# Kernel tuning notes

Hardware: AMD Instinct MI355X
Metric: run time of the kernel (lower is better)

Reference implementation:

```python
import jax, jax.numpy as jnp
import numpy as np

N_TOKENS = 3
EMBED = 10
RNN = 10
N_LABELS = 3
B = 16384
T = 99
EPS = 1e-7  # keras CategoricalCrossentropy clip epsilon


def setup_inputs() -> dict:
    key = jax.random.key(0)
    ks = jax.random.split(key, 8)
    token_ids = jax.random.randint(ks[0], (B, T), 0, N_TOKENS, dtype=jnp.int32)
    label_ids = jax.random.randint(ks[1], (B, T), 0, N_LABELS)
    labels = jax.nn.one_hot(label_ids, N_LABELS, dtype=jnp.float32)
    mask = jnp.ones((B, T), dtype=bool)  # accepted by call() but unused, kept for signature fidelity
    emb_table = jax.random.normal(ks[2], (N_TOKENS, EMBED), jnp.float32) * 0.05
    W = jax.random.normal(ks[3], (EMBED, RNN), jnp.float32) / np.sqrt(EMBED)
    U = jax.random.normal(ks[4], (RNN, RNN), jnp.float32) / np.sqrt(RNN)
    b = jnp.zeros((RNN,), jnp.float32)
    Wo = jax.random.normal(ks[5], (RNN, N_LABELS), jnp.float32) / np.sqrt(RNN)
    bo = jnp.zeros((N_LABELS,), jnp.float32)
    return dict(token_ids=token_ids, labels=labels, mask=mask,
                emb_table=emb_table, W=W, U=U, b=b, Wo=Wo, bo=bo)


def reference(token_ids, labels, mask, emb_table, W, U, b, Wo, bo):
    # Embedding lookup (mask_zero=True -> token 0 is a masked step)
    emb = emb_table[token_ids]                      # [B, T, E]
    step_mask = (token_ids != 0)                    # [B, T]

    def step(h, inp):
        x_t, m_t = inp                              # [B, E], [B]
        h_new = jnp.tanh(x_t @ W + h @ U + b)       # SimpleRNN cell
        # Keras masking: masked timesteps carry previous state/output
        h = jnp.where(m_t[:, None], h_new, h)
        return h, h

    h0 = jnp.zeros((token_ids.shape[0], W.shape[1]), emb.dtype)
    _, states_tb = jax.lax.scan(step, h0, (emb.transpose(1, 0, 2), step_mask.T))
    states = states_tb.transpose(1, 0, 2)           # [B, T, R]

    probs = jax.nn.softmax(states @ Wo + bo, axis=-1)   # Dense(softmax) -> [B, T, L]
    probs_c = jnp.clip(probs, EPS, 1.0)
    loss = jnp.mean(-jnp.sum(labels * jnp.log(probs_c), axis=-1))
    accuracy = jnp.mean((jnp.argmax(probs, axis=-1) == jnp.argmax(labels, axis=-1)).astype(jnp.float32))
    return states, probs, accuracy, loss
```

## Files before the change

### kernel.cpp

```cpp
#include <hip/hip_runtime.h>
#include <math.h>

#define BB 16384
#define TT 99
#define RR 10
#define LL 3
#define TILE 33
#define RPW 8
#define WPB 4

#define QP(v, j) __int_as_float(__builtin_amdgcn_mov_dpp(                     \
    __float_as_int(v), (j) * 0x55, 0xF, 0xF, true))
#define HMIR(v)  __int_as_float(__builtin_amdgcn_mov_dpp(                     \
    __float_as_int(v), 0x141, 0xF, 0xF, true))

__device__ __forceinline__ float fast_tanh(float x) {
    float e = __expf(2.0f * x);
    return fmaf(-2.0f, __builtin_amdgcn_rcpf(e + 1.0f), 1.0f);
}

__global__ __launch_bounds__(256, 2)
void rnn_fused_kernel(const int* __restrict__ tok_ids,
                      const float* __restrict__ labels,
                      const float* __restrict__ emb,
                      const float* __restrict__ W,
                      const float* __restrict__ U,
                      const float* __restrict__ bvec,
                      const float* __restrict__ Wo,
                      const float* __restrict__ bo,
                      float* __restrict__ states_out,
                      float* __restrict__ probs_out,
                      float* __restrict__ ws)
{
    __shared__ __align__(16) float          s_st[WPB][RPW * TILE * RR];
    __shared__                unsigned char s_code[WPB][RPW * 100];

    const int tid = threadIdx.x;
    const int w   = tid >> 6;
    const int l   = tid & 63;
    const int r8  = l >> 3;
    const int g   = l & 7;
    const int rowbase = blockIdx.x * (WPB * RPW) + w * RPW;

#pragma unroll 1
    for (int i = 0; i < 13; ++i) {
        const int p = l + 64 * i;
        if (p < RPW * TT) {
            const size_t gi = (size_t)rowbase * TT + p;
            const int   tk  = tok_ids[gi];
            const float la1 = labels[gi * LL + 1];
            const float la2 = labels[gi * LL + 2];
            const int   y   = (la1 > 0.5f) ? 1 : ((la2 > 0.5f) ? 2 : 0);
            const int   r   = p / TT;
            s_code[w][r * 100 + (p - r * TT)] = (unsigned char)((tk << 2) | y);
        }
    }

    const int qpar = g >> 2;
    int ord[8];
#pragma unroll
    for (int j = 0; j < 4; ++j) {
        ord[j]     = qpar ? 4 + j : j;
        ord[4 + j] = qpar ? 3 - j : 7 - j;
    }
    const int jA = g;
    const int jB = ((g & 3) < 2) ? 8 + (g & 3) : 8;

    float UA[RR], UB[RR];
#pragma unroll
    for (int k2 = 0; k2 < 8; ++k2) {
        UA[k2] = U[ord[k2] * RR + jA];
        UB[k2] = U[ord[k2] * RR + jB];
    }
    UA[8] = U[8 * RR + jA]; UA[9] = U[9 * RR + jA];
    UB[8] = U[8 * RR + jB]; UB[9] = U[9 * RR + jB];

    float cA1 = bvec[jA], cA2 = cA1, cB1 = bvec[jB], cB2 = cB1;
#pragma unroll
    for (int i = 0; i < RR; ++i) {
        const float e1 = emb[RR + i];
        const float e2 = emb[2 * RR + i];
        const float wA = W[i * RR + jA];
        const float wB = W[i * RR + jB];
        cA1 = fmaf(e1, wA, cA1); cA2 = fmaf(e2, wA, cA2);
        cB1 = fmaf(e1, wB, cB1); cB2 = fmaf(e2, wB, cB2);
    }

    float hoA = 0.0f, hoB = 0.0f;
    float loss = 0.0f;
    int   corr = 0;
    int code = (int)s_code[w][r8 * 100];

#pragma unroll 1
    for (int k = 0; k < 3; ++k) {
#pragma unroll 1
        for (int tt = 0; tt < TILE; ++tt) {
            const int t   = k * TILE + tt;
            const int cur = code;
            const int tn  = (t + 1 < TT) ? t + 1 : t;
            code = (int)s_code[w][r8 * 100 + tn];
            const int sel = cur >> 2;

            float hg[RR];
            hg[0] = QP(hoA, 0); hg[1] = QP(hoA, 1);
            hg[2] = QP(hoA, 2); hg[3] = QP(hoA, 3);
            const float mr = HMIR(hoA);
            hg[4] = QP(mr, 0);  hg[5] = QP(mr, 1);
            hg[6] = QP(mr, 2);  hg[7] = QP(mr, 3);
            hg[8] = QP(hoB, 0); hg[9] = QP(hoB, 1);

            const bool is1 = (sel == 1);
            float aA0 = is1 ? cA1 : cA2, aB0 = is1 ? cB1 : cB2;
            float aA1 = 0.0f, aB1 = 0.0f;
#pragma unroll
            for (int i = 0; i < 5; ++i) {
                aA0 = fmaf(hg[i],     UA[i],     aA0);
                aA1 = fmaf(hg[5 + i], UA[5 + i], aA1);
                aB0 = fmaf(hg[i],     UB[i],     aB0);
                aB1 = fmaf(hg[5 + i], UB[5 + i], aB1);
            }
            const float hnA = fast_tanh(aA0 + aA1);
            const float hnB = fast_tanh(aB0 + aB1);
            if (sel != 0) { hoA = hnA; hoB = hnB; }

            float* sp = &s_st[w][(r8 * TILE + tt) * RR];
            sp[g] = hoA;
            if (g < 2) sp[8 + g] = hoB;
        }

#pragma unroll 1
        for (int i = 0; i < 21; ++i) {
            const int p = l + 64 * i;
            if (p < 1320) {
                const int r = p / 165;
                const int m = p - r * 165;
                const float2 v = *reinterpret_cast<const float2*>(
                    &s_st[w][r * (TILE * RR) + 2 * m]);
                *reinterpret_cast<float2*>(
                    &states_out[(size_t)(rowbase + r) * (TT * RR)
                                + (size_t)k * (TILE * RR) + 2 * m]) = v;
            }
        }

#pragma unroll 1
        for (int i = 0; i < 5; ++i) {
            const int p = l + 64 * i;
            if (p < RPW * TILE) {
                const int r  = p / TILE;
                const int t2 = p - r * TILE;
                const size_t idx = (size_t)(rowbase + r) * TT + k * TILE + t2;

                const float* hp = &s_st[w][(r * TILE + t2) * RR];
                float h0[RR];
#pragma unroll
                for (int j = 0; j < RR; j += 2) {
                    const float2 v = *reinterpret_cast<const float2*>(hp + j);
                    h0[j] = v.x; h0[j + 1] = v.y;
                }
                float l0 = bo[0], l1 = bo[1], l2 = bo[2];
#pragma unroll
                for (int j = 0; j < RR; ++j) {
                    l0 = fmaf(h0[j], Wo[j * LL + 0], l0);
                    l1 = fmaf(h0[j], Wo[j * LL + 1], l1);
                    l2 = fmaf(h0[j], Wo[j * LL + 2], l2);
                }
                const float e0 = __expf(l0), e1 = __expf(l1), e2 = __expf(l2);
                const float S  = e0 + e1 + e2;
                const float rs = __builtin_amdgcn_rcpf(S);
                probs_out[idx * LL + 0] = e0 * rs;
                probs_out[idx * LL + 1] = e1 * rs;
                probs_out[idx * LL + 2] = e2 * rs;

                const int y = (int)s_code[w][r * 100 + k * TILE + t2] & 3;

                const float ly = (y == 0) ? l0 : ((y == 1) ? l1 : l2);
                loss += fminf(__logf(S) - ly, 16.11809565f);

                int ap = 0; float pm = l0;
                if (l1 > pm) { ap = 1; pm = l1; }
                if (l2 > pm) { ap = 2; }
                corr += (ap == y) ? 1 : 0;
            }
        }
    }

    float ls = loss, cs = (float)corr;
#pragma unroll
    for (int off = 32; off > 0; off >>= 1) {
        ls += __shfl_down(ls, off, 64);
        cs += __shfl_down(cs, off, 64);
    }
    if (l == 0) {
        const int wid = blockIdx.x * WPB + w;
        ws[wid]        = ls;
        ws[2048 + wid] = cs;
    }
}

__global__ __launch_bounds__(256)
void finalize_kernel(const float* __restrict__ ws, float* __restrict__ out_tail)
{
    __shared__ float sl[4], sc[4];
    const int t = threadIdx.x;
    float ls = 0.0f, cs = 0.0f;
#pragma unroll
    for (int i = 0; i < 8; ++i) {
        ls += ws[t + 256 * i];
        cs += ws[2048 + t + 256 * i];
    }
#pragma unroll
    for (int off = 32; off > 0; off >>= 1) {
        ls += __shfl_down(ls, off, 64);
        cs += __shfl_down(cs, off, 64);
    }
    if ((t & 63) == 0) { sl[t >> 6] = ls; sc[t >> 6] = cs; }
    __syncthreads();
    if (t == 0) {
        const float L = sl[0] + sl[1] + sl[2] + sl[3];
        const float C = sc[0] + sc[1] + sc[2] + sc[3];
        const float inv = 1.0f / (float)((size_t)BB * TT);
        out_tail[0] = C * inv;
        out_tail[1] = L * inv;
    }
}

extern "C" void kernel_launch(void* const* d_in, const int* in_sizes, int n_in,
                              void* d_out, int out_size, void* d_ws, size_t ws_size,
                              hipStream_t stream)
{
    const int*   tok    = (const int*)  d_in[0];
    const float* labels = (const float*)d_in[1];
    const float* emb = (const float*)d_in[3];
    const float* W   = (const float*)d_in[4];
    const float* U   = (const float*)d_in[5];
    const float* bv  = (const float*)d_in[6];
    const float* Wo  = (const float*)d_in[7];
    const float* bo  = (const float*)d_in[8];

    float* out    = (float*)d_out;
    float* states = out;
    float* probs  = out + (size_t)BB * TT * RR;
    float* tail   = out + (size_t)BB * TT * (RR + LL);
    float* ws     = (float*)d_ws;

    rnn_fused_kernel<<<BB / (WPB * RPW), 256, 0, stream>>>(
        tok, labels, emb, W, U, bv, Wo, bo, states, probs, ws);
    finalize_kernel<<<1, 256, 0, stream>>>(ws, tail);
}
```

Before: 51.11 us.

## Split fused RNN into recurrence kernel and separate dense/softmax epilogue kernel

Replaces the single fused kernel with a recurrence-only kernel that writes hidden states straight to global memory, plus a grid-stride epilogue kernel. The epilogue re-reads states and labels to compute probs, loss and accuracy. The point is to take the LDS staging, tiled copy-out and per-tile softmax work off the serial recurrence's critical path and to run the epilogue at full parallelism. The cost is an extra round trip of the states tensor through global memory, an extra launch, and scattered 4-byte state stores from the recurrence.

New measurement: 49.64 us. 1.03x faster.

```diff
diff --git a/kernel.cpp b/kernel.cpp
--- a/kernel.cpp
+++ b/kernel.cpp
@@ -5,9 +5,6 @@
 #define TT 99
 #define RR 10
 #define LL 3
-#define TILE 33
-#define RPW 8
-#define WPB 4
 
 #define QP(v, j) __int_as_float(__builtin_amdgcn_mov_dpp(                     \
     __float_as_int(v), (j) * 0x55, 0xF, 0xF, true))
@@ -20,39 +17,29 @@
 }
 
 __global__ __launch_bounds__(256, 2)
-void rnn_fused_kernel(const int* __restrict__ tok_ids,
-                      const float* __restrict__ labels,
-                      const float* __restrict__ emb,
-                      const float* __restrict__ W,
-                      const float* __restrict__ U,
-                      const float* __restrict__ bvec,
-                      const float* __restrict__ Wo,
-                      const float* __restrict__ bo,
-                      float* __restrict__ states_out,
-                      float* __restrict__ probs_out,
-                      float* __restrict__ ws)
-{
-    __shared__ __align__(16) float          s_st[WPB][RPW * TILE * RR];
-    __shared__                unsigned char s_code[WPB][RPW * 100];
+void rnn_seq_kernel(const int* __restrict__ tok_ids,
+                    const float* __restrict__ emb,
+                    const float* __restrict__ W,
+                    const float* __restrict__ U,
+                    const float* __restrict__ bvec,
+                    float* __restrict__ states_out)
+{
+    __shared__ unsigned char s_tk[4][8 * 100];
 
     const int tid = threadIdx.x;
     const int w   = tid >> 6;
     const int l   = tid & 63;
     const int r8  = l >> 3;
     const int g   = l & 7;
-    const int rowbase = blockIdx.x * (WPB * RPW) + w * RPW;
-
-#pragma unroll 1
+    const int rowbase = blockIdx.x * 32 + w * 8;
+
+#pragma unroll
     for (int i = 0; i < 13; ++i) {
         const int p = l + 64 * i;
-        if (p < RPW * TT) {
-            const size_t gi = (size_t)rowbase * TT + p;
-            const int   tk  = tok_ids[gi];
-            const float la1 = labels[gi * LL + 1];
-            const float la2 = labels[gi * LL + 2];
-            const int   y   = (la1 > 0.5f) ? 1 : ((la2 > 0.5f) ? 2 : 0);
-            const int   r   = p / TT;
-            s_code[w][r * 100 + (p - r * TT)] = (unsigned char)((tk << 2) | y);
+        if (p < 8 * TT) {
+            const int r = p / TT;
+            s_tk[w][r * 100 + (p - r * TT)] =
+                (unsigned char)tok_ids[(size_t)rowbase * TT + p];
         }
     }
 
@@ -87,113 +74,116 @@
     }
 
     float hoA = 0.0f, hoB = 0.0f;
+    float* outA = states_out + (size_t)(rowbase + r8) * (TT * RR) + jA;
+    float* outB = states_out + (size_t)(rowbase + r8) * (TT * RR) + jB;
+
+    int code = (int)s_tk[w][r8 * 100];
+
+#pragma unroll 11
+    for (int t = 0; t < TT; ++t) {
+        const int cur = code;
+        const int tn  = (t + 1 < TT) ? t + 1 : t;
+        code = (int)s_tk[w][r8 * 100 + tn];
+
+        float hg[RR];
+        hg[0] = QP(hoA, 0); hg[1] = QP(hoA, 1);
+        hg[2] = QP(hoA, 2); hg[3] = QP(hoA, 3);
+        const float mr = HMIR(hoA);
+        hg[4] = QP(mr, 0);  hg[5] = QP(mr, 1);
+        hg[6] = QP(mr, 2);  hg[7] = QP(mr, 3);
+        hg[8] = QP(hoB, 0); hg[9] = QP(hoB, 1);
+
+        const bool is1 = (cur == 1);
+        float aA0 = is1 ? cA1 : cA2, aB0 = is1 ? cB1 : cB2;
+        float aA1 = 0.0f, aB1 = 0.0f;
+#pragma unroll
+        for (int i = 0; i < 5; ++i) {
+            aA0 = fmaf(hg[i],     UA[i],     aA0);
+            aA1 = fmaf(hg[5 + i], UA[5 + i], aA1);
+            aB0 = fmaf(hg[i],     UB[i],     aB0);
+            aB1 = fmaf(hg[5 + i], UB[5 + i], aB1);
+        }
+        const float hnA = fast_tanh(aA0 + aA1);
+        const float hnB = fast_tanh(aB0 + aB1);
+        if (cur != 0) { hoA = hnA; hoB = hnB; }
+
+        outA[t * RR] = hoA;
+        outB[t * RR] = hoB;
+    }
+}
+
+__global__ __launch_bounds__(256)
+void epilogue_kernel(const float* __restrict__ states,
+                     const float* __restrict__ labels,
+                     const float* __restrict__ Wo,
+                     const float* __restrict__ bo,
+                     float* __restrict__ probs_out,
+                     float* __restrict__ ws)
+{
+    const int NT     = BB * TT;
+    const int tid    = blockIdx.x * 256 + threadIdx.x;
+    const int stride = 2048 * 256;
+
+    float Wc0[RR], Wc1[RR], Wc2[RR];
+#pragma unroll
+    for (int j = 0; j < RR; ++j) {
+        Wc0[j] = Wo[j * LL + 0];
+        Wc1[j] = Wo[j * LL + 1];
+        Wc2[j] = Wo[j * LL + 2];
+    }
+    const float b0 = bo[0], b1 = bo[1], b2 = bo[2];
+
     float loss = 0.0f;
     int   corr = 0;
-    int code = (int)s_code[w][r8 * 100];
 
 #pragma unroll 1
-    for (int k = 0; k < 3; ++k) {
-#pragma unroll 1
-        for (int tt = 0; tt < TILE; ++tt) {
-            const int t   = k * TILE + tt;
-            const int cur = code;
-            const int tn  = (t + 1 < TT) ? t + 1 : t;
-            code = (int)s_code[w][r8 * 100 + tn];
-            const int sel = cur >> 2;
-
-            float hg[RR];
-            hg[0] = QP(hoA, 0); hg[1] = QP(hoA, 1);
-            hg[2] = QP(hoA, 2); hg[3] = QP(hoA, 3);
-            const float mr = HMIR(hoA);
-            hg[4] = QP(mr, 0);  hg[5] = QP(mr, 1);
-            hg[6] = QP(mr, 2);  hg[7] = QP(mr, 3);
-            hg[8] = QP(hoB, 0); hg[9] = QP(hoB, 1);
-
-            const bool is1 = (sel == 1);
-            float aA0 = is1 ? cA1 : cA2, aB0 = is1 ? cB1 : cB2;
-            float aA1 = 0.0f, aB1 = 0.0f;
-#pragma unroll
-            for (int i = 0; i < 5; ++i) {
-                aA0 = fmaf(hg[i],     UA[i],     aA0);
-                aA1 = fmaf(hg[5 + i], UA[5 + i], aA1);
-                aB0 = fmaf(hg[i],     UB[i],     aB0);
-                aB1 = fmaf(hg[5 + i], UB[5 + i], aB1);
-            }
-            const float hnA = fast_tanh(aA0 + aA1);
-            const float hnB = fast_tanh(aB0 + aB1);
-            if (sel != 0) { hoA = hnA; hoB = hnB; }
-
-            float* sp = &s_st[w][(r8 * TILE + tt) * RR];
-            sp[g] = hoA;
-            if (g < 2) sp[8 + g] = hoB;
-        }
-
-#pragma unroll 1
-        for (int i = 0; i < 21; ++i) {
-            const int p = l + 64 * i;
-            if (p < 1320) {
-                const int r = p / 165;
-                const int m = p - r * 165;
-                const float2 v = *reinterpret_cast<const float2*>(
-                    &s_st[w][r * (TILE * RR) + 2 * m]);
-                *reinterpret_cast<float2*>(
-                    &states_out[(size_t)(rowbase + r) * (TT * RR)
-                                + (size_t)k * (TILE * RR) + 2 * m]) = v;
-            }
-        }
-
-#pragma unroll 1
-        for (int i = 0; i < 5; ++i) {
-            const int p = l + 64 * i;
-            if (p < RPW * TILE) {
-                const int r  = p / TILE;
-                const int t2 = p - r * TILE;
-                const size_t idx = (size_t)(rowbase + r) * TT + k * TILE + t2;
-
-                const float* hp = &s_st[w][(r * TILE + t2) * RR];
-                float h0[RR];
-#pragma unroll
-                for (int j = 0; j < RR; j += 2) {
-                    const float2 v = *reinterpret_cast<const float2*>(hp + j);
-                    h0[j] = v.x; h0[j + 1] = v.y;
-                }
-                float l0 = bo[0], l1 = bo[1], l2 = bo[2];
-#pragma unroll
-                for (int j = 0; j < RR; ++j) {
-                    l0 = fmaf(h0[j], Wo[j * LL + 0], l0);
-                    l1 = fmaf(h0[j], Wo[j * LL + 1], l1);
-                    l2 = fmaf(h0[j], Wo[j * LL + 2], l2);
-                }
-                const float e0 = __expf(l0), e1 = __expf(l1), e2 = __expf(l2);
-                const float S  = e0 + e1 + e2;
-                const float rs = __builtin_amdgcn_rcpf(S);
-                probs_out[idx * LL + 0] = e0 * rs;
-                probs_out[idx * LL + 1] = e1 * rs;
-                probs_out[idx * LL + 2] = e2 * rs;
-
-                const int y = (int)s_code[w][r * 100 + k * TILE + t2] & 3;
-
-                const float ly = (y == 0) ? l0 : ((y == 1) ? l1 : l2);
-                loss += fminf(__logf(S) - ly, 16.11809565f);
-
-                int ap = 0; float pm = l0;
-                if (l1 > pm) { ap = 1; pm = l1; }
-                if (l2 > pm) { ap = 2; }
-                corr += (ap == y) ? 1 : 0;
-            }
-        }
-    }
-
+    for (int idx = tid; idx < NT; idx += stride) {
+        const float* hp = states + (size_t)idx * RR;
+        float h[RR];
+#pragma unroll
+        for (int j = 0; j < RR; j += 2) {
+            const float2 v = *reinterpret_cast<const float2*>(hp + j);
+            h[j] = v.x; h[j + 1] = v.y;
+        }
+        const float la1 = labels[(size_t)idx * LL + 1];
+        const float la2 = labels[(size_t)idx * LL + 2];
+        const int   y   = (la1 > 0.5f) ? 1 : ((la2 > 0.5f) ? 2 : 0);
+
+        float l0 = b0, l1 = b1, l2 = b2;
+#pragma unroll
+        for (int j = 0; j < RR; ++j) {
+            l0 = fmaf(h[j], Wc0[j], l0);
+            l1 = fmaf(h[j], Wc1[j], l1);
+            l2 = fmaf(h[j], Wc2[j], l2);
+        }
+        const float e0 = __expf(l0), e1 = __expf(l1), e2 = __expf(l2);
+        const float S  = e0 + e1 + e2;
+        const float rs = __builtin_amdgcn_rcpf(S);
+        probs_out[(size_t)idx * LL + 0] = e0 * rs;
+        probs_out[(size_t)idx * LL + 1] = e1 * rs;
+        probs_out[(size_t)idx * LL + 2] = e2 * rs;
+
+        const float ly = (y == 0) ? l0 : ((y == 1) ? l1 : l2);
+        loss += fminf(__logf(S) - ly, 16.11809565f);
+
+        int ap = 0; float pm = l0;
+        if (l1 > pm) { ap = 1; pm = l1; }
+        if (l2 > pm) { ap = 2; }
+        corr += (ap == y) ? 1 : 0;
+    }
+
+    __shared__ float sl[4], sc[4];
     float ls = loss, cs = (float)corr;
 #pragma unroll
     for (int off = 32; off > 0; off >>= 1) {
         ls += __shfl_down(ls, off, 64);
         cs += __shfl_down(cs, off, 64);
     }
-    if (l == 0) {
-        const int wid = blockIdx.x * WPB + w;
-        ws[wid]        = ls;
-        ws[2048 + wid] = cs;
+    if ((threadIdx.x & 63) == 0) { sl[threadIdx.x >> 6] = ls; sc[threadIdx.x >> 6] = cs; }
+    __syncthreads();
+    if (threadIdx.x == 0) {
+        ws[blockIdx.x]        = sl[0] + sl[1] + sl[2] + sl[3];
+        ws[2048 + blockIdx.x] = sc[0] + sc[1] + sc[2] + sc[3];
     }
 }
 
@@ -243,7 +233,7 @@
     float* tail   = out + (size_t)BB * TT * (RR + LL);
     float* ws     = (float*)d_ws;
 
-    rnn_fused_kernel<<<BB / (WPB * RPW), 256, 0, stream>>>(
-        tok, labels, emb, W, U, bv, Wo, bo, states, probs, ws);
+    rnn_seq_kernel<<<512, 256, 0, stream>>>(tok, emb, W, U, bv, states);
+    epilogue_kernel<<<2048, 256, 0, stream>>>(states, labels, Wo, bo, probs, ws);
     finalize_kernel<<<1, 256, 0, stream>>>(ws, tail);
 }
```
